# Kernel tuning notes

Measured on AMD Instinct MI355X. Metric: run time of the kernel, lower is better.

## Reference

```python
import jax, jax.numpy as jnp
import numpy as np

B, H, W, DIM = 64, 28, 28, 384
N = B * H * W
E, K, R = 3, 2, 8
HID = 4 * DIM
SCALING = 8.0 / 8.0  # alpha / r


def setup_inputs() -> dict:
    key = jax.random.key(0)
    ks = jax.random.split(key, 8)
    x = jax.random.normal(ks[0], (B, H, W, DIM), dtype=jnp.float32)
    gate = jax.random.uniform(ks[1], (N, E), dtype=jnp.float32)
    topk_probs = jax.random.uniform(ks[2], (N, K), dtype=jnp.float32)
    topk_idx = jax.random.randint(ks[3], (N, K), 0, E)
    # LoRA expert params (w_up is zeros in the original init; use small randn
    # so the MoE path is numerically non-trivial for kernel testing)
    w_down = jax.random.normal(ks[4], (E, DIM, R), dtype=jnp.float32) * (1.0 / DIM ** 0.5)
    w_up = jax.random.normal(ks[5], (E, R, DIM), dtype=jnp.float32) * 0.02
    # frozen base ConvNeXt MLP: Linear(dim,4dim) -> GELU -> Linear(4dim,dim)
    W1 = jax.random.normal(ks[6], (DIM, HID), dtype=jnp.float32) * 0.02
    b1 = jnp.zeros((HID,), dtype=jnp.float32)
    W2 = jax.random.normal(ks[7], (HID, DIM), dtype=jnp.float32) * 0.02
    b2 = jnp.zeros((DIM,), dtype=jnp.float32)
    return {"x": x, "gate": gate, "topk_probs": topk_probs, "topk_idx": topk_idx,
            "w_down": w_down, "w_up": w_up, "W1": W1, "b1": b1, "W2": W2, "b2": b2}


def reference(x, gate, topk_probs, topk_idx, w_down, w_up, W1, b1, W2, b2):
    gelu = lambda t: jax.nn.gelu(t, approximate=False)  # torch nn.GELU() default = exact erf
    # frozen base MLP
    orig = gelu(jnp.einsum('bhwd,df->bhwf', x, W1) + b1)
    orig = jnp.einsum('bhwf,fd->bhwd', orig, W2) + b2
    # MoE LoRA path over flattened tokens
    x_flat = x.reshape(-1, x.shape[-1])          # [N, dim]
    moe = jnp.zeros_like(x_flat)
    n_experts = w_down.shape[0]
    for i in range(n_experts):
        # combined routing weight for expert i (0 for tokens not routed here)
        prob = jnp.sum(jnp.where(topk_idx == i, topk_probs, 0.0), axis=1)  # [N]
        out_i = gelu(x_flat @ w_down[i]) @ w_up[i] * SCALING               # [N, dim]
        moe = moe + out_i * prob[:, None]
    return orig + moe.reshape(x.shape)
```

## Files before the change

kernel.cpp:

```cpp
#include <hip/hip_runtime.h>
#include <hip/hip_bf16.h>

typedef __attribute__((ext_vector_type(4))) float float4v;
typedef __attribute__((ext_vector_type(8))) __bf16 bf16x8;
typedef __attribute__((ext_vector_type(8))) unsigned short ushort8v;

constexpr int NTOK = 50176;
constexpr int DIM  = 384;
constexpr int HID  = 1536;
constexpr int BM   = 64;
constexpr int NTH  = 512;
constexpr int NBLK = NTOK / BM;
constexpr int CHW  = 32;
constexpr int NCH  = HID / CHW;

constexpr int IMG_WD  = 0;
constexpr int IMG_WUP = 24576;
constexpr int IMG_W1  = 49152;
constexpr int IMG_W2  = 49152 + 48 * 24576;
constexpr size_t WS_NEED = 2408448;
constexpr int NELEMS = 1204224;

constexpr int L_X  = 0;
constexpr int L_W  = 49152;
constexpr int L_HS = 73728;
constexpr int LDSZ = 77824;

__device__ __forceinline__ unsigned short f2bf(float f) {
  __hip_bfloat16 h = __float2bfloat16(f);
  return *reinterpret_cast<unsigned short*>(&h);
}

__device__ __forceinline__ float gelu_f(float v) {
  float u = 0.7978845608f * (v + 0.044715f * v * v * v);
  float e = __expf(2.0f * u);
  float t = 1.0f - 2.0f / (e + 1.0f);
  return 0.5f * v * (1.0f + t);
}

__device__ __forceinline__ int gt_addr(int r, int s) {
  return ((r >> 3) << 9) + (s << 7) + ((r & 7) << 4);
}

__device__ __forceinline__ void st_load(const char* src, int tid, ushort8v st[3]) {
  #pragma unroll
  for (int j = 0; j < 3; ++j)
    st[j] = *(const ushort8v*)(src + tid * 16 + j * 8192);
}
__device__ __forceinline__ void st_wr(char* dst, int tid, const ushort8v st[3]) {
  #pragma unroll
  for (int j = 0; j < 3; ++j)
    *(ushort8v*)(dst + tid * 16 + j * 8192) = st[j];
}

__global__ __launch_bounds__(256) void pack_k(
    const float* __restrict__ W1, const float* __restrict__ W2,
    const float* __restrict__ wd, const float* __restrict__ wu,
    unsigned short* __restrict__ img)
{
  int i = blockIdx.x * 256 + threadIdx.x;
  if (i >= NELEMS) return;
  if (i < 12288) {
    int f = i / 384; int inb = (i % 384) * 2;
    int d = (inb ^ ((f & 7) << 4)) >> 1;
    float v = (f < 24) ? wd[(f >> 3) * (DIM * 8) + d * 8 + (f & 7)] : 0.f;
    img[i] = f2bf(v);
  } else if (i < 24576) {
    int j = i - 12288;
    int d = (j >> 8) * 8 + ((j >> 3) & 7);
    int k = ((j >> 6) & 3) * 8 + (j & 7);
    float v = (k < 24) ? wu[k * DIM + d] : 0.f;
    img[i] = f2bf(v);
  } else if (i < 24576 + 48 * 12288) {
    int j = i - 24576; int h = j / 12288; int jc = j % 12288;
    int f = jc / 384; int inb = (jc % 384) * 2;
    int d = (inb ^ ((f & 7) << 4)) >> 1;
    img[i] = f2bf(W1[d * HID + h * CHW + f]);
  } else {
    int j = i - 24576 - 48 * 12288; int h = j / 12288; int jc = j % 12288;
    int d = (jc >> 8) * 8 + ((jc >> 3) & 7);
    int k = ((jc >> 6) & 3) * 8 + (jc & 7);
    img[i] = f2bf(W2[(h * CHW + k) * DIM + d]);
  }
}

__global__ __launch_bounds__(NTH, 4) void fused_k(
    const float* __restrict__ x,
    const float* __restrict__ tp,
    const int*   __restrict__ ti,
    const float* __restrict__ b1,
    const float* __restrict__ b2,
    const unsigned short* __restrict__ img,
    float* __restrict__ out)
{
  extern __shared__ char lds[];
  const int tid = threadIdx.x, wid = tid >> 6, lane = tid & 63;
  const int lrow = lane & 15, g4 = lane >> 4;
  const int blockRow = blockIdx.x * BM;
  const char* imgc = (const char*)img;

  const int band = wid >> 1, chh = wid & 1;
  const int wr = wid >> 2, wc = wid & 3;

  ushort8v st[3];

  st_load(imgc + IMG_WD, tid, st);
  {
    const float* xb = x + (size_t)blockRow * DIM;
    #pragma unroll
    for (int it = 0; it < 6; ++it) {
      int idx = it * NTH + tid;
      int row = idx / 48, c8 = idx % 48;
      float4v v0 = *(const float4v*)(xb + row * DIM + c8 * 8);
      float4v v1 = *(const float4v*)(xb + row * DIM + c8 * 8 + 4);
      ushort8v u;
      u[0]=f2bf(v0[0]); u[1]=f2bf(v0[1]); u[2]=f2bf(v0[2]); u[3]=f2bf(v0[3]);
      u[4]=f2bf(v1[0]); u[5]=f2bf(v1[1]); u[6]=f2bf(v1[2]); u[7]=f2bf(v1[3]);
      int byte = (row * 768 + c8 * 16) ^ ((row & 7) << 4);
      *(ushort8v*)(lds + L_X + byte) = u;
    }
  }
  __syncthreads();
  st_wr(lds + L_W, tid, st);
  __syncthreads();
  st_load(imgc + IMG_WUP, tid, st);

  {
    float4v hv = {};
    int raX = band * 16 + lrow, sA = (raX & 7) << 4, baX = raX * 768 + g4 * 16;
    int rbW = chh * 16 + lrow, sB = (rbW & 7) << 4, baW = rbW * 768 + g4 * 16;
    #pragma unroll
    for (int ks = 0; ks < 12; ++ks) {
      bf16x8 a = *(const bf16x8*)(lds + L_X + ((baX + ks * 64) ^ sA));
      bf16x8 b = *(const bf16x8*)(lds + L_W + ((baW + ks * 64) ^ sB));
      hv = __builtin_amdgcn_mfma_f32_16x16x32_bf16(a, b, hv, 0, 0, 0);
    }
    int colc = chh * 16 + lrow; int e = colc >> 3;
    #pragma unroll
    for (int r = 0; r < 4; ++r) {
      int row = band * 16 + g4 * 4 + r;
      int token = blockRow + row;
      float p = 0.f;
      if (e < 3) {
        int i0 = ti[token * 2], i1 = ti[token * 2 + 1];
        if (i0 == e) p += tp[token * 2];
        if (i1 == e) p += tp[token * 2 + 1];
      }
      float gv = p * gelu_f(hv[r]);
      int byte = gt_addr(row, colc >> 3) + ((colc & 7) << 1);
      *(unsigned short*)(lds + L_HS + byte) = f2bf(gv);
    }
  }
  __syncthreads();
  st_wr(lds + L_W, tid, st);
  __syncthreads();
  st_load(imgc + IMG_W1, tid, st);

  float4v acc[2][6] = {};
  {
    bf16x8 A[2];
    #pragma unroll
    for (int mt = 0; mt < 2; ++mt) {
      int ra = wr * 32 + mt * 16 + lrow;
      A[mt] = *(const bf16x8*)(lds + L_HS + gt_addr(ra, g4));
    }
    #pragma unroll
    for (int nt = 0; nt < 6; ++nt) {
      int rd = wc * 96 + nt * 16 + lrow;
      bf16x8 b = *(const bf16x8*)(lds + L_W + gt_addr(rd, g4));
      acc[0][nt] = __builtin_amdgcn_mfma_f32_16x16x32_bf16(A[0], b, acc[0][nt], 0, 0, 0);
      acc[1][nt] = __builtin_amdgcn_mfma_f32_16x16x32_bf16(A[1], b, acc[1][nt], 0, 0, 0);
    }
  }

  for (int h = 0; h < NCH; ++h) {
    __syncthreads();
    st_wr(lds + L_W, tid, st);
    __syncthreads();
    st_load(imgc + IMG_W2 + h * 24576, tid, st);

    float4v hv = {};
    {
      int raX = band * 16 + lrow, sA = (raX & 7) << 4, baX = raX * 768 + g4 * 16;
      int rbW = chh * 16 + lrow, sB = (rbW & 7) << 4, baW = rbW * 768 + g4 * 16;
      #pragma unroll
      for (int ks = 0; ks < 12; ++ks) {
        bf16x8 a = *(const bf16x8*)(lds + L_X + ((baX + ks * 64) ^ sA));
        bf16x8 b = *(const bf16x8*)(lds + L_W + ((baW + ks * 64) ^ sB));
        hv = __builtin_amdgcn_mfma_f32_16x16x32_bf16(a, b, hv, 0, 0, 0);
      }
    }
    {
      int colc = chh * 16 + lrow;
      float bb = b1[h * CHW + colc];
      #pragma unroll
      for (int r = 0; r < 4; ++r) {
        int row = band * 16 + g4 * 4 + r;
        float gv = gelu_f(hv[r] + bb);
        int byte = gt_addr(row, colc >> 3) + ((colc & 7) << 1);
        *(unsigned short*)(lds + L_HS + byte) = f2bf(gv);
      }
    }
    __syncthreads();
    st_wr(lds + L_W, tid, st);
    __syncthreads();
    if (h < NCH - 1)
      st_load(imgc + IMG_W1 + (h + 1) * 24576, tid, st);

    {
      bf16x8 A[2];
      #pragma unroll
      for (int mt = 0; mt < 2; ++mt) {
        int ra = wr * 32 + mt * 16 + lrow;
        A[mt] = *(const bf16x8*)(lds + L_HS + gt_addr(ra, g4));
      }
      #pragma unroll
      for (int nt = 0; nt < 6; ++nt) {
        int rd = wc * 96 + nt * 16 + lrow;
        bf16x8 b = *(const bf16x8*)(lds + L_W + gt_addr(rd, g4));
        acc[0][nt] = __builtin_amdgcn_mfma_f32_16x16x32_bf16(A[0], b, acc[0][nt], 0, 0, 0);
        acc[1][nt] = __builtin_amdgcn_mfma_f32_16x16x32_bf16(A[1], b, acc[1][nt], 0, 0, 0);
      }
    }
  }

  #pragma unroll
  for (int nt = 0; nt < 6; ++nt) {
    int col = wc * 96 + nt * 16 + lrow;
    float bb = b2[col];
    #pragma unroll
    for (int mt = 0; mt < 2; ++mt) {
      #pragma unroll
      for (int r = 0; r < 4; ++r) {
        int row = wr * 32 + mt * 16 + g4 * 4 + r;
        out[(size_t)(blockRow + row) * DIM + col] = acc[mt][nt][r] + bb;
      }
    }
  }
}

extern "C" void kernel_launch(void* const* d_in, const int* in_sizes, int n_in,
                              void* d_out, int out_size, void* d_ws, size_t ws_size,
                              hipStream_t stream) {
  const float* x          = (const float*)d_in[0];
  const float* topk_probs = (const float*)d_in[2];
  const int*   topk_idx   = (const int*)  d_in[3];
  const float* w_down     = (const float*)d_in[4];
  const float* w_up       = (const float*)d_in[5];
  const float* W1         = (const float*)d_in[6];
  const float* b1         = (const float*)d_in[7];
  const float* W2         = (const float*)d_in[8];
  const float* b2         = (const float*)d_in[9];
  float* out = (float*)d_out;

  if (ws_size < WS_NEED) return;

  hipFuncSetAttribute(reinterpret_cast<const void*>(fused_k),
                      hipFuncAttributeMaxDynamicSharedMemorySize, LDSZ);

  unsigned short* img = (unsigned short*)d_ws;
  pack_k<<<(NELEMS + 255) / 256, 256, 0, stream>>>(W1, W2, w_down, w_up, img);
  fused_k<<<NBLK, NTH, LDSZ, stream>>>(x, topk_probs, topk_idx, b1, b2, img, out);
}
```

Before: 284.1 us.

## Read W2/Wup fragments directly from global memory and double-buffer hidden LDS tile

The W2 and W_up packed images are relaid as contiguous per-column 32-element rows, so each wave loads its MFMA B fragments straight from global/L2 into registers instead of staging them through LDS. The hidden-activation buffer is double-buffered (LDS grows by 4 KB), which allows two __syncthreads per chunk to be dropped, leaving only W1 staged through LDS. The goal is to cut LDS traffic and barrier count in the main loop, at the cost of more global/L2 loads per wave and more register pressure.

```diff
diff --git a/kernel.cpp b/kernel.cpp
--- a/kernel.cpp
+++ b/kernel.cpp
@@ -17,14 +17,14 @@
 constexpr int IMG_WD  = 0;
 constexpr int IMG_WUP = 24576;
 constexpr int IMG_W1  = 49152;
-constexpr int IMG_W2  = 49152 + 48 * 24576;
+constexpr int IMG_W2  = 49152 + 48 * 12288 * 2;
 constexpr size_t WS_NEED = 2408448;
 constexpr int NELEMS = 1204224;
 
 constexpr int L_X  = 0;
 constexpr int L_W  = 49152;
 constexpr int L_HS = 73728;
-constexpr int LDSZ = 77824;
+constexpr int LDSZ = 81920;
 
 __device__ __forceinline__ unsigned short f2bf(float f) {
   __hip_bfloat16 h = __float2bfloat16(f);
@@ -67,9 +67,8 @@
     img[i] = f2bf(v);
   } else if (i < 24576) {
     int j = i - 12288;
-    int d = (j >> 8) * 8 + ((j >> 3) & 7);
-    int k = ((j >> 6) & 3) * 8 + (j & 7);
-    float v = (k < 24) ? wu[k * DIM + d] : 0.f;
+    int d = j / 32, c = j % 32;
+    float v = (c < 24) ? wu[c * DIM + d] : 0.f;
     img[i] = f2bf(v);
   } else if (i < 24576 + 48 * 12288) {
     int j = i - 24576; int h = j / 12288; int jc = j % 12288;
@@ -78,8 +77,7 @@
     img[i] = f2bf(W1[d * HID + h * CHW + f]);
   } else {
     int j = i - 24576 - 48 * 12288; int h = j / 12288; int jc = j % 12288;
-    int d = (jc >> 8) * 8 + ((jc >> 3) & 7);
-    int k = ((jc >> 6) & 3) * 8 + (jc & 7);
+    int d = jc / 32, k = jc % 32;
     img[i] = f2bf(W2[(h * CHW + k) * DIM + d]);
   }
 }
@@ -120,10 +118,9 @@
       *(ushort8v*)(lds + L_X + byte) = u;
     }
   }
+  st_wr(lds + L_W, tid, st);
+  st_load(imgc + IMG_W1, tid, st);
   __syncthreads();
-  st_wr(lds + L_W, tid, st);
-  __syncthreads();
-  st_load(imgc + IMG_WUP, tid, st);
 
   {
     float4v hv = {};
@@ -153,11 +150,15 @@
   }
   __syncthreads();
   st_wr(lds + L_W, tid, st);
-  __syncthreads();
-  st_load(imgc + IMG_W1, tid, st);
 
   float4v acc[2][6] = {};
   {
+    bf16x8 bfr[6];
+    #pragma unroll
+    for (int nt = 0; nt < 6; ++nt) {
+      int rd = wc * 96 + nt * 16 + lrow;
+      bfr[nt] = *(const bf16x8*)(imgc + IMG_WUP + rd * 64 + g4 * 16);
+    }
     bf16x8 A[2];
     #pragma unroll
     for (int mt = 0; mt < 2; ++mt) {
@@ -166,18 +167,16 @@
     }
     #pragma unroll
     for (int nt = 0; nt < 6; ++nt) {
-      int rd = wc * 96 + nt * 16 + lrow;
-      bf16x8 b = *(const bf16x8*)(lds + L_W + gt_addr(rd, g4));
-      acc[0][nt] = __builtin_amdgcn_mfma_f32_16x16x32_bf16(A[0], b, acc[0][nt], 0, 0, 0);
-      acc[1][nt] = __builtin_amdgcn_mfma_f32_16x16x32_bf16(A[1], b, acc[1][nt], 0, 0, 0);
+      acc[0][nt] = __builtin_amdgcn_mfma_f32_16x16x32_bf16(A[0], bfr[nt], acc[0][nt], 0, 0, 0);
+      acc[1][nt] = __builtin_amdgcn_mfma_f32_16x16x32_bf16(A[1], bfr[nt], acc[1][nt], 0, 0, 0);
     }
   }
 
   for (int h = 0; h < NCH; ++h) {
+    const int hb = 4096 - ((h & 1) << 12);
     __syncthreads();
-    st_wr(lds + L_W, tid, st);
-    __syncthreads();
-    st_load(imgc + IMG_W2 + h * 24576, tid, st);
+    if (h < NCH - 1)
+      st_load(imgc + IMG_W1 + (h + 1) * 24576, tid, st);
 
     float4v hv = {};
     {
@@ -198,28 +197,31 @@
         int row = band * 16 + g4 * 4 + r;
         float gv = gelu_f(hv[r] + bb);
         int byte = gt_addr(row, colc >> 3) + ((colc & 7) << 1);
-        *(unsigned short*)(lds + L_HS + byte) = f2bf(gv);
-      }
-    }
-    __syncthreads();
-    st_wr(lds + L_W, tid, st);
+        *(unsigned short*)(lds + L_HS + hb + byte) = f2bf(gv);
+      }
+    }
     __syncthreads();
     if (h < NCH - 1)
-      st_load(imgc + IMG_W1 + (h + 1) * 24576, tid, st);
+      st_wr(lds + L_W, tid, st);
 
     {
+      const char* w2b = imgc + IMG_W2 + h * 24576;
+      bf16x8 bfr[6];
+      #pragma unroll
+      for (int nt = 0; nt < 6; ++nt) {
+        int rd = wc * 96 + nt * 16 + lrow;
+        bfr[nt] = *(const bf16x8*)(w2b + rd * 64 + g4 * 16);
+      }
       bf16x8 A[2];
       #pragma unroll
       for (int mt = 0; mt < 2; ++mt) {
         int ra = wr * 32 + mt * 16 + lrow;
-        A[mt] = *(const bf16x8*)(lds + L_HS + gt_addr(ra, g4));
+        A[mt] = *(const bf16x8*)(lds + L_HS + hb + gt_addr(ra, g4));
       }
       #pragma unroll
       for (int nt = 0; nt < 6; ++nt) {
-        int rd = wc * 96 + nt * 16 + lrow;
-        bf16x8 b = *(const bf16x8*)(lds + L_W + gt_addr(rd, g4));
-        acc[0][nt] = __builtin_amdgcn_mfma_f32_16x16x32_bf16(A[0], b, acc[0][nt], 0, 0, 0);
-        acc[1][nt] = __builtin_amdgcn_mfma_f32_16x16x32_bf16(A[1], b, acc[1][nt], 0, 0, 0);
+        acc[0][nt] = __builtin_amdgcn_mfma_f32_16x16x32_bf16(A[0], bfr[nt], acc[0][nt], 0, 0, 0);
+        acc[1][nt] = __builtin_amdgcn_mfma_f32_16x16x32_bf16(A[1], bfr[nt], acc[1][nt], 0, 0, 0);
       }
     }
   }
```

Result: faster. 276.9 us (-2.5%).
